# Kernel tuning notes

Measured on AMD Instinct MI355X. Metric: run time of the kernel, lower is better.

## Reference

```python
import jax, jax.numpy as jnp
import numpy as np

D_MODEL = 1024
N_HEADS = 16
D_KV = 64
ROPE_THETA = 10000.0


def setup_inputs() -> dict:
    key = jax.random.key(0)
    k1, k2, k3, k4, k5 = jax.random.split(key, 5)
    B, S = 4, 2048
    scale = 0.02
    return {
        "positions": jnp.arange(S, dtype=jnp.int64 if jax.config.jax_enable_x64 else jnp.int32),
        "hidden_states": jax.random.normal(k1, (B, S, D_MODEL), dtype=jnp.float32),
        "wq": jax.random.normal(k2, (D_MODEL, N_HEADS * D_KV), dtype=jnp.float32) * scale,
        "wk": jax.random.normal(k3, (D_MODEL, N_HEADS * D_KV), dtype=jnp.float32) * scale,
        "wv": jax.random.normal(k4, (D_MODEL, N_HEADS * D_KV), dtype=jnp.float32) * scale,
        "wo": jax.random.normal(k5, (N_HEADS * D_KV, D_MODEL), dtype=jnp.float32) * scale,
    }


def _rope(positions, q, k):
    # Neox-style simple RoPE, matching SimpleRoPE fallback.
    # q, k: [B, H, S, Dh]
    Dh = q.shape[-1]
    inv_freq = 1.0 / (ROPE_THETA ** (jnp.arange(0, Dh, 2, dtype=jnp.float32) / Dh))  # [Dh/2]
    freqs = positions.astype(jnp.float32)[:, None] * inv_freq[None, :]  # [S, Dh/2]
    emb = jnp.concatenate([freqs, freqs], axis=-1)  # [S, Dh]
    cos = jnp.cos(emb)[None, None, :, :]
    sin = jnp.sin(emb)[None, None, :, :]

    def rotate_half(x):
        x1, x2 = jnp.split(x, 2, axis=-1)
        return jnp.concatenate([-x2, x1], axis=-1)

    q_rot = q * cos + rotate_half(q) * sin
    k_rot = k * cos + rotate_half(k) * sin
    return q_rot, k_rot


def reference(positions, hidden_states, wq, wk, wv, wo):
    B, S, _ = hidden_states.shape
    H, Dh = N_HEADS, D_KV

    def split_heads(x):  # [B, S, H*Dh] -> [B, H, S, Dh]
        return x.reshape(B, S, H, Dh).transpose(0, 2, 1, 3)

    q = split_heads(hidden_states @ wq)
    k = split_heads(hidden_states @ wk)
    v = split_heads(hidden_states @ wv)

    q, k = _rope(positions, q, k)

    # scale = 1.0 (no 1/sqrt(d) scaling), matching the source module
    scores = jnp.einsum("bhqd,bhkd->bhqk", q, k)
    attn = jax.nn.softmax(scores.astype(jnp.float32), axis=-1).astype(scores.dtype)
    # dropout is identity in eval mode
    out = jnp.einsum("bhqk,bhkd->bhqd", attn, v)  # [B, H, S, Dh]
    out = out.transpose(0, 2, 1, 3).reshape(B, S, H * Dh)
    return out @ wo
```

## Files before the change

### kernel.cpp

```cpp
#include <hip/hip_runtime.h>
#include <hip/hip_bf16.h>


typedef __bf16 bf16_t;
typedef __bf16 bf16x4 __attribute__((ext_vector_type(4)));
typedef __bf16 bf16x8 __attribute__((ext_vector_type(8)));
typedef float f32x4 __attribute__((ext_vector_type(4)));

#define MFMA16(a, b, c) __builtin_amdgcn_mfma_f32_16x16x32_bf16((a), (b), (c), 0, 0, 0)

#define GLOAD_LDS(gp, lp) \
  __builtin_amdgcn_global_load_lds( \
      (const __attribute__((address_space(1))) void*)(gp), \
      (__attribute__((address_space(3))) void*)(lp), 16, 0, 0)

__global__ __launch_bounds__(256) void cvt_kernel(const float* __restrict__ X,
                                                  bf16_t* __restrict__ Y) {
  const int i = (blockIdx.x * 256 + threadIdx.x) * 4;
  const f32x4 x = *(const f32x4*)(X + i);
  bf16x4 y;
#pragma unroll
  for (int k = 0; k < 4; k++) y[k] = (bf16_t)x[k];
  *(bf16x4*)(Y + i) = y;
}

__global__ __launch_bounds__(256) void wtrans4_kernel(
    const float* __restrict__ w0, const float* __restrict__ w1,
    const float* __restrict__ w2, const float* __restrict__ w3,
    bf16_t* __restrict__ out) {
  __shared__ bf16_t t[32][33];
  const int tx = threadIdx.x, ty = threadIdx.y;
  const int bx = blockIdx.x, by = blockIdx.y, z = blockIdx.z;
  const float* W = (z == 0) ? w0 : (z == 1) ? w1 : (z == 2) ? w2 : w3;
  bf16_t* Wt = out + (size_t)z * 1024 * 1024;
#pragma unroll
  for (int i = ty; i < 32; i += 8)
    t[i][tx] = (bf16_t)W[(size_t)(by * 32 + i) * 1024 + bx * 32 + tx];
  __syncthreads();
#pragma unroll
  for (int i = ty; i < 32; i += 8)
    Wt[(size_t)(bx * 32 + i) * 1024 + by * 32 + tx] = t[tx][i];
}

__global__ __launch_bounds__(256) void vtrans_kernel(const bf16_t* __restrict__ V,
                                                     bf16_t* __restrict__ VT) {
  __shared__ bf16_t t[32][33];
  const int tx = threadIdx.x, ty = threadIdx.y;
  const int sx = blockIdx.x * 32, cy = blockIdx.y * 32, b = blockIdx.z;
  const bf16_t* Vb = V + (size_t)b * 2048 * 1024;
  bf16_t* VTb = VT + (size_t)b * 1024 * 2048;
#pragma unroll
  for (int i = ty; i < 32; i += 8)
    t[i][tx] = Vb[(size_t)(sx + i) * 1024 + cy + tx];
  __syncthreads();
#pragma unroll
  for (int i = ty; i < 32; i += 8)
    VTb[(size_t)(cy + i) * 2048 + sx + tx] = t[tx][i];
}

template <typename TC, bool FUSED_QKV>
__global__ __launch_bounds__(256) void gemm_kernel(
    const bf16_t* __restrict__ A, const bf16_t* __restrict__ BtBase,
    TC* __restrict__ CBase, const int ropeIn) {
  constexpr int K = 1024, N = 1024;
  __shared__ __align__(16) bf16_t As[128 * 32];
  __shared__ __align__(16) bf16_t Bs[128 * 32];

  const int tid = threadIdx.x;
  const int lane = tid & 63, w = tid >> 6;
  const int l15 = lane & 15, quad = lane >> 4;
  const int wm = w >> 1, wn = w & 1;
  const int m0 = blockIdx.x * 128;

  int n0, rope;
  const bf16_t* Bt;
  TC* C;
  if (FUSED_QKV) {
    const int which = blockIdx.y >> 3;
    n0 = (blockIdx.y & 7) * 128;
    Bt = BtBase + (size_t)which * (1u << 20);
    C = CBase + (size_t)which * (8u << 20);
    rope = (which < 2);
  } else {
    n0 = blockIdx.y * 128;
    Bt = BtBase;
    C = CBase;
    rope = ropeIn;
  }

  f32x4 acc[4][4] = {};
  const int li8 = lane >> 3, j = lane & 7;

  for (int k0 = 0; k0 < K; k0 += 32) {
#pragma unroll
    for (int p = 0; p < 2; ++p) {
      const int g = w * 16 + p * 8 + li8;
      const int jp = j ^ (g & 7);
      const int row = 2 * g + (jp >> 2), kb = jp & 3;
      GLOAD_LDS(A + (size_t)(m0 + row) * K + k0 + kb * 8, As + (w * 16 + p * 8) * 64);
      GLOAD_LDS(Bt + (size_t)(n0 + row) * K + k0 + kb * 8, Bs + (w * 16 + p * 8) * 64);
    }
    __syncthreads();

    bf16x8 af[4], bfv[4];
#pragma unroll
    for (int mi = 0; mi < 4; mi++) {
      const int R = wm * 64 + mi * 16 + l15, g = R >> 1;
      const int jj = (((R & 1) << 2) | quad) ^ (g & 7);
      af[mi] = *(const bf16x8*)(As + g * 64 + jj * 8);
    }
#pragma unroll
    for (int ni = 0; ni < 4; ni++) {
      const int R = wn * 64 + ni * 16 + l15, g = R >> 1;
      const int jj = (((R & 1) << 2) | quad) ^ (g & 7);
      bfv[ni] = *(const bf16x8*)(Bs + g * 64 + jj * 8);
    }
#pragma unroll
    for (int mi = 0; mi < 4; mi++)
#pragma unroll
      for (int ni = 0; ni < 4; ni++)
        acc[mi][ni] = MFMA16(af[mi], bfv[ni], acc[mi][ni]);
    __syncthreads();
  }

#pragma unroll
  for (int mi = 0; mi < 4; mi++) {
    const int rbase = m0 + wm * 64 + mi * 16 + quad * 4;
    if (rope) {
#pragma unroll
      for (int r = 0; r < 4; r++) {
        const float pos = (float)((rbase + r) & 2047);
#pragma unroll
        for (int ni = 0; ni < 2; ni++) {
          const int d2 = ni * 16 + l15;
          const float invf = __powf(10000.0f, -(float)d2 * (1.0f / 32.0f));
          float sv, cv;
          __sincosf(pos * invf, &sv, &cv);
          const float a0 = acc[mi][ni][r], a2 = acc[mi][ni + 2][r];
          acc[mi][ni][r] = a0 * cv - a2 * sv;
          acc[mi][ni + 2][r] = a2 * cv + a0 * sv;
        }
      }
    }
#pragma unroll
    for (int ni = 0; ni < 4; ni++) {
      const int c0 = n0 + wn * 64 + ni * 16 + l15;
#pragma unroll
      for (int r = 0; r < 4; r++)
        C[(size_t)(rbase + r) * N + c0] = (TC)acc[mi][ni][r];
    }
  }
}

#define PSTR 72

__global__ __launch_bounds__(256) void attn_kernel(const bf16_t* __restrict__ Q,
                                                   const bf16_t* __restrict__ K,
                                                   const bf16_t* __restrict__ VT,
                                                   bf16_t* __restrict__ O) {
  __shared__ __align__(16) bf16_t Kl[64 * 64];
  __shared__ __align__(16) bf16_t Vl[64 * 64];
  __shared__ __align__(16) bf16_t Pl[4 * 16 * PSTR];

  const int tid = threadIdx.x;
  const int lane = tid & 63, w = tid >> 6;
  const int l15 = lane & 15, quad = lane >> 4;
  const int q0 = blockIdx.x * 64;
  const int bh = blockIdx.y, b = bh >> 4, h = bh & 15;

  const size_t base = (size_t)b * 2048 * 1024 + (size_t)h * 64;
  const bf16_t* Qb = Q + base;
  const bf16_t* Kb = K + base;
  const bf16_t* VTb = VT + (size_t)(b * 1024 + h * 64) * 2048;

  const int qrow = q0 + w * 16 + l15;
  bf16x8 qf[2];
  qf[0] = *(const bf16x8*)(Qb + (size_t)qrow * 1024 + quad * 8);
  qf[1] = *(const bf16x8*)(Qb + (size_t)qrow * 1024 + 32 + quad * 8);

  f32x4 accO[4] = {};
  float lsum[4] = {0.f, 0.f, 0.f, 0.f};

  const int li8 = lane >> 3, j = lane & 7;

  for (int kv0 = 0; kv0 < 2048; kv0 += 64) {
#pragma unroll
    for (int p = 0; p < 2; ++p) {
      const int kr = w * 16 + p * 8 + li8;
      const int blk = j ^ (kr & 7);
      GLOAD_LDS(Kb + (size_t)(kv0 + kr) * 1024 + blk * 8, Kl + (w * 16 + p * 8) * 64);
      GLOAD_LDS(VTb + (size_t)kr * 2048 + kv0 + blk * 8, Vl + (w * 16 + p * 8) * 64);
    }
    __syncthreads();

    f32x4 sc[4] = {};
#pragma unroll
    for (int t = 0; t < 2; t++)
#pragma unroll
      for (int nb = 0; nb < 4; nb++) {
        const int R = nb * 16 + l15;
        const int jj = (t * 4 + quad) ^ (R & 7);
        const bf16x8 kf = *(const bf16x8*)(Kl + R * 64 + jj * 8);
        sc[nb] = MFMA16(qf[t], kf, sc[nb]);
      }

#pragma unroll
    for (int nb = 0; nb < 4; nb++)
#pragma unroll
      for (int r = 0; r < 4; r++) {
        const float p = __expf(sc[nb][r]);
        lsum[r] += p;
        Pl[w * 16 * PSTR + (quad * 4 + r) * PSTR + nb * 16 + l15] = (bf16_t)p;
      }
    __asm__ volatile("s_waitcnt lgkmcnt(0)" ::: "memory");

#pragma unroll
    for (int t = 0; t < 2; t++) {
      const bf16x8 pf = *(const bf16x8*)(Pl + w * 16 * PSTR + l15 * PSTR + t * 32 + quad * 8);
#pragma unroll
      for (int nb = 0; nb < 4; nb++) {
        const int R = nb * 16 + l15;
        const int jj = (t * 4 + quad) ^ (R & 7);
        const bf16x8 vf = *(const bf16x8*)(Vl + R * 64 + jj * 8);
        accO[nb] = MFMA16(pf, vf, accO[nb]);
      }
    }
    __syncthreads();
  }

#pragma unroll
  for (int r = 0; r < 4; r++) {
    float s = lsum[r];
    s += __shfl_xor(s, 1);
    s += __shfl_xor(s, 2);
    s += __shfl_xor(s, 4);
    s += __shfl_xor(s, 8);
    lsum[r] = 1.0f / s;
  }
  bf16_t* Ob = O + base;
#pragma unroll
  for (int r = 0; r < 4; r++) {
    const int qr = q0 + w * 16 + quad * 4 + r;
#pragma unroll
    for (int nb = 0; nb < 4; nb++)
      Ob[(size_t)qr * 1024 + nb * 16 + l15] = (bf16_t)(accO[nb][r] * lsum[r]);
  }
}

extern "C" void kernel_launch(void* const* d_in, const int* in_sizes, int n_in,
                              void* d_out, int out_size, void* d_ws, size_t ws_size,
                              hipStream_t stream) {
  const float* hs = (const float*)d_in[1];
  const float* wq = (const float*)d_in[2];
  const float* wk = (const float*)d_in[3];
  const float* wv = (const float*)d_in[4];
  const float* wo = (const float*)d_in[5];

  char* ws = (char*)d_ws;
  const size_t MB = 1024 * 1024;
  bf16_t* WtQKV = (bf16_t*)(ws + 0 * MB);
  bf16_t* WtO = (bf16_t*)(ws + 6 * MB);
  bf16_t* hsb = (bf16_t*)(ws + 8 * MB);
  bf16_t* VT = (bf16_t*)(ws + 8 * MB);
  bf16_t* Qw = (bf16_t*)(ws + 24 * MB);
  bf16_t* Kw = (bf16_t*)(ws + 40 * MB);
  bf16_t* Vw = (bf16_t*)(ws + 56 * MB);
  bf16_t* Ow = (bf16_t*)(ws + 56 * MB);

  wtrans4_kernel<<<dim3(32, 32, 4), dim3(32, 8), 0, stream>>>(wq, wk, wv, wo, WtQKV);
  cvt_kernel<<<8192, 256, 0, stream>>>(hs, hsb);

  gemm_kernel<bf16_t, true><<<dim3(64, 24), 256, 0, stream>>>(hsb, WtQKV, Qw, 0);

  vtrans_kernel<<<dim3(64, 32, 4), dim3(32, 8), 0, stream>>>(Vw, VT);

  attn_kernel<<<dim3(32, 64), 256, 0, stream>>>(Qw, Kw, VT, Ow);

  gemm_kernel<float, false><<<dim3(64, 8), 256, 0, stream>>>(Ow, WtO, (float*)d_out, 0);
}
```

Before: 341.5 us.

## Double-buffer K/V tiles in attention and remap blocks across XCDs

The attention kernel now keeps two LDS buffers for K and V and prefetches the next KV tile while computing on the current one, waiting on vmcnt instead of a full barrier sync. It also remaps block indices so that consecutive blocks are spread across the 8 compute dies, which is meant to improve L2 reuse of K/V. The P tile is staged in two halves with a smaller stride, and s_setprio is raised around the MFMA sections. In exchange the kernel uses more LDS, which may reduce occupancy, and the correctness of the raw vmcnt/barrier ordering depends on the hand-written waits.

```diff
diff --git a/kernel.cpp b/kernel.cpp
--- a/kernel.cpp
+++ b/kernel.cpp
@@ -152,28 +152,31 @@
   }
 }
 
-#define PSTR 72
+#define PSTR 48
 
 __global__ __launch_bounds__(256) void attn_kernel(const bf16_t* __restrict__ Q,
                                                    const bf16_t* __restrict__ K,
                                                    const bf16_t* __restrict__ VT,
                                                    bf16_t* __restrict__ O) {
-  __shared__ __align__(16) bf16_t Kl[64 * 64];
-  __shared__ __align__(16) bf16_t Vl[64 * 64];
+  __shared__ __align__(16) bf16_t Kl[2][64 * 64];
+  __shared__ __align__(16) bf16_t Vl[2][64 * 64];
   __shared__ __align__(16) bf16_t Pl[4 * 16 * PSTR];
 
   const int tid = threadIdx.x;
-  const int lane = tid & 63, w = tid >> 6;
+  const int lane = tid & 63, wv = tid >> 6;
   const int l15 = lane & 15, quad = lane >> 4;
-  const int q0 = blockIdx.x * 64;
-  const int bh = blockIdx.y, b = bh >> 4, h = bh & 15;
+
+  const int orig = blockIdx.y * 32 + blockIdx.x;
+  const int wk = (orig & 7) * 256 + (orig >> 3);
+  const int q0 = (wk & 31) * 64;
+  const int bh = wk >> 5, b = bh >> 4, h = bh & 15;
 
   const size_t base = (size_t)b * 2048 * 1024 + (size_t)h * 64;
   const bf16_t* Qb = Q + base;
   const bf16_t* Kb = K + base;
   const bf16_t* VTb = VT + (size_t)(b * 1024 + h * 64) * 2048;
 
-  const int qrow = q0 + w * 16 + l15;
+  const int qrow = q0 + wv * 16 + l15;
   bf16x8 qf[2];
   qf[0] = *(const bf16x8*)(Qb + (size_t)qrow * 1024 + quad * 8);
   qf[1] = *(const bf16x8*)(Qb + (size_t)qrow * 1024 + 32 + quad * 8);
@@ -183,49 +186,63 @@
 
   const int li8 = lane >> 3, j = lane & 7;
 
-  for (int kv0 = 0; kv0 < 2048; kv0 += 64) {
+  auto stage = [&](int buf, int kvb) {
 #pragma unroll
     for (int p = 0; p < 2; ++p) {
-      const int kr = w * 16 + p * 8 + li8;
+      const int kr = wv * 16 + p * 8 + li8;
       const int blk = j ^ (kr & 7);
-      GLOAD_LDS(Kb + (size_t)(kv0 + kr) * 1024 + blk * 8, Kl + (w * 16 + p * 8) * 64);
-      GLOAD_LDS(VTb + (size_t)kr * 2048 + kv0 + blk * 8, Vl + (w * 16 + p * 8) * 64);
-    }
-    __syncthreads();
+      GLOAD_LDS(Kb + (size_t)(kvb + kr) * 1024 + blk * 8, &Kl[buf][(wv * 16 + p * 8) * 64]);
+      GLOAD_LDS(VTb + (size_t)kr * 2048 + kvb + blk * 8, &Vl[buf][(wv * 16 + p * 8) * 64]);
+    }
+  };
+
+  stage(0, 0);
+  for (int t = 0; t < 32; ++t) {
+    const int cur = t & 1;
+    if (t < 31) {
+      stage(cur ^ 1, (t + 1) * 64);
+      __asm__ volatile("s_waitcnt vmcnt(4)" ::: "memory");
+    } else {
+      __asm__ volatile("s_waitcnt vmcnt(0)" ::: "memory");
+    }
+    __builtin_amdgcn_s_barrier();
 
     f32x4 sc[4] = {};
-#pragma unroll
-    for (int t = 0; t < 2; t++)
+    __builtin_amdgcn_s_setprio(1);
+#pragma unroll
+    for (int tt = 0; tt < 2; tt++)
 #pragma unroll
       for (int nb = 0; nb < 4; nb++) {
         const int R = nb * 16 + l15;
-        const int jj = (t * 4 + quad) ^ (R & 7);
-        const bf16x8 kf = *(const bf16x8*)(Kl + R * 64 + jj * 8);
-        sc[nb] = MFMA16(qf[t], kf, sc[nb]);
+        const int jj = (tt * 4 + quad) ^ (R & 7);
+        const bf16x8 kf = *(const bf16x8*)(&Kl[cur][R * 64 + jj * 8]);
+        sc[nb] = MFMA16(qf[tt], kf, sc[nb]);
       }
-
-#pragma unroll
-    for (int nb = 0; nb < 4; nb++)
-#pragma unroll
-      for (int r = 0; r < 4; r++) {
-        const float p = __expf(sc[nb][r]);
-        lsum[r] += p;
-        Pl[w * 16 * PSTR + (quad * 4 + r) * PSTR + nb * 16 + l15] = (bf16_t)p;
-      }
-    __asm__ volatile("s_waitcnt lgkmcnt(0)" ::: "memory");
-
-#pragma unroll
-    for (int t = 0; t < 2; t++) {
-      const bf16x8 pf = *(const bf16x8*)(Pl + w * 16 * PSTR + l15 * PSTR + t * 32 + quad * 8);
+    __builtin_amdgcn_s_setprio(0);
+
+#pragma unroll
+    for (int hf = 0; hf < 2; hf++) {
+#pragma unroll
+      for (int nb2 = 0; nb2 < 2; nb2++)
+#pragma unroll
+        for (int r = 0; r < 4; r++) {
+          const float p = __expf(sc[hf * 2 + nb2][r]);
+          lsum[r] += p;
+          Pl[wv * 16 * PSTR + (quad * 4 + r) * PSTR + nb2 * 16 + l15] = (bf16_t)p;
+        }
+      __asm__ volatile("s_waitcnt lgkmcnt(0)" ::: "memory");
+      const bf16x8 pf = *(const bf16x8*)(&Pl[wv * 16 * PSTR + l15 * PSTR + quad * 8]);
+      __builtin_amdgcn_s_setprio(1);
 #pragma unroll
       for (int nb = 0; nb < 4; nb++) {
         const int R = nb * 16 + l15;
-        const int jj = (t * 4 + quad) ^ (R & 7);
-        const bf16x8 vf = *(const bf16x8*)(Vl + R * 64 + jj * 8);
+        const int jj = (hf * 4 + quad) ^ (R & 7);
+        const bf16x8 vf = *(const bf16x8*)(&Vl[cur][R * 64 + jj * 8]);
         accO[nb] = MFMA16(pf, vf, accO[nb]);
       }
-    }
-    __syncthreads();
+      __builtin_amdgcn_s_setprio(0);
+    }
+    __builtin_amdgcn_s_barrier();
   }
 
 #pragma unroll
@@ -240,7 +257,7 @@
   bf16_t* Ob = O + base;
 #pragma unroll
   for (int r = 0; r < 4; r++) {
-    const int qr = q0 + w * 16 + quad * 4 + r;
+    const int qr = q0 + wv * 16 + quad * 4 + r;
 #pragma unroll
     for (int nb = 0; nb < 4; nb++)
       Ob[(size_t)qr * 1024 + nb * 16 + l15] = (bf16_t)(accO[nb][r] * lsum[r]);
```

Result: no change. 341.3 us, median of 2 (-0.1%).
